# Performance work log

Measured on AMD Instinct MI355X. Metric: run time of the kernel, lower is better.

The kernel has to match this reference:

```python
import jax, jax.numpy as jnp
import numpy as np

# config (matches SS2Dv2 defaults: d_model=96, d_state=16, ssm_ratio=2.0, dt_rank=auto=6, k_group=4)
DM, DI, N, K, R = 96, 192, 16, 4, 6
BSZ, H_, W_ = 1, 56, 56


def setup_inputs() -> dict:
    key = jax.random.key(0)
    ks = jax.random.split(key, 8)
    return {
        "x": jax.random.normal(ks[0], (BSZ, H_, W_, DM), jnp.float32),
        "in_proj_w": jax.random.normal(ks[1], (2 * DI, DM), jnp.float32) / np.sqrt(DM).astype(np.float32),
        "conv_w": jax.random.normal(ks[2], (DI, 1, 3, 3), jnp.float32) * 0.1,
        "conv_b": jnp.zeros((DI,), jnp.float32),
        "x_proj_w": jax.random.normal(ks[3], (K, R + 2 * N, DI), jnp.float32) / np.sqrt(DI).astype(np.float32),
        "dt_projs_w": 0.1 * jax.random.uniform(ks[4], (K, DI, R), jnp.float32),
        "dt_projs_bias": 0.1 * jax.random.uniform(ks[5], (K, DI), jnp.float32),
        "A_logs": jnp.zeros((K * DI, N), jnp.float32),
        "Ds": jnp.ones((K * DI,), jnp.float32),
        "ln_w": jnp.ones((DI,), jnp.float32),
        "ln_b": jnp.zeros((DI,), jnp.float32),
        "out_proj_w": jax.random.normal(ks[6], (DM, DI), jnp.float32) / np.sqrt(DI).astype(np.float32),
    }


def _cross_scan(x):
    # x: (B, D, H, W) -> (B, 4, D, L); dirs: row-major, col-major, and their flips
    B, D, H, W = x.shape
    L = H * W
    x0 = x.reshape(B, D, L)
    x1 = jnp.swapaxes(x, 2, 3).reshape(B, D, L)
    return jnp.stack([x0, x1, x0[..., ::-1], x1[..., ::-1]], axis=1)


def _cross_merge(ys, H, W):
    # ys: (B, K, D, L) -> (B, D, L); invert each scan direction and sum
    B, Kk, D, L = ys.shape
    y0 = ys[:, 0]
    y2 = ys[:, 2][..., ::-1]
    y1 = jnp.swapaxes(ys[:, 1].reshape(B, D, W, H), 2, 3).reshape(B, D, L)
    y3 = jnp.swapaxes(ys[:, 3][..., ::-1].reshape(B, D, W, H), 2, 3).reshape(B, D, L)
    return y0 + y1 + y2 + y3


def _forward(x, in_proj_w, conv_w, conv_b, x_proj_w, dt_projs_w, dt_projs_bias,
             A_logs, Ds, ln_w, ln_b, out_proj_w):
    B, H, W, _ = x.shape
    L = H * W
    # in_proj + gate split (channel_first=False -> last dim)
    xz = jnp.einsum('bhwc,oc->bhwo', x, in_proj_w)
    xc, z = jnp.split(xz, 2, axis=-1)
    z = jax.nn.silu(z)
    # depthwise conv (NCHW)
    xc = jnp.transpose(xc, (0, 3, 1, 2))
    xc = jax.lax.conv_general_dilated(
        xc, conv_w, (1, 1), 'SAME', feature_group_count=DI,
        dimension_numbers=('NCHW', 'OIHW', 'NCHW')) + conv_b[None, :, None, None]
    xc = jax.nn.silu(xc)
    # 4-directional cross scan
    xs = _cross_scan(xc)  # (B,K,D,L)
    # grouped x_proj: per direction D -> R+2N
    x_dbl = jnp.einsum('bkdl,krd->bkrl', xs, x_proj_w)
    dts, Bs, Cs = jnp.split(x_dbl, [R, R + N], axis=2)  # (B,K,R,L),(B,K,N,L),(B,K,N,L)
    # grouped dt proj: per direction R -> D
    dts = jnp.einsum('bkrl,kdr->bkdl', dts, dt_projs_w)
    A = -jnp.exp(A_logs.astype(jnp.float32)).reshape(K, DI, N)
    delta = jax.nn.softplus(dts + dt_projs_bias[None, :, :, None])  # (B,K,D,L)
    # S6 selective scan: h_t = exp(delta*A)*h_{t-1} + delta*B*u, y_t = C.h_t + D*u
    dA = jnp.exp(jnp.einsum('bkdl,kdn->bkdln', delta, A))
    dBu = jnp.einsum('bkdl,bknl,bkdl->bkdln', delta, Bs, xs)

    def comb(e1, e2):
        a1, b1 = e1
        a2, b2 = e2
        return a2 * a1, a2 * b1 + b2

    _, h = jax.lax.associative_scan(comb, (dA, dBu), axis=3)  # (B,K,D,L,N)
    y = jnp.einsum('bkdln,bknl->bkdl', h, Cs) + Ds.reshape(K, DI)[None, :, :, None] * xs
    y = _cross_merge(y, H, W).reshape(B, DI, H, W)
    # out_norm: LayerNorm over channels (channel_first=False path)
    y = jnp.transpose(y, (0, 2, 3, 1))  # (B,H,W,D)
    mu = y.mean(-1, keepdims=True)
    var = ((y - mu) ** 2).mean(-1, keepdims=True)
    y = (y - mu) / jnp.sqrt(var + 1e-5) * ln_w + ln_b
    y = y * z
    return jnp.einsum('bhwd,od->bhwo', y, out_proj_w)


def reference(x, in_proj_w, conv_w, conv_b, x_proj_w, dt_projs_w, dt_projs_bias,
              A_logs, Ds, ln_w, ln_b, out_proj_w):
    return _forward(x, in_proj_w, conv_w, conv_b, x_proj_w, dt_projs_w, dt_projs_bias,
                    A_logs, Ds, ln_w, ln_b, out_proj_w)
```

## Files before the change

kernel.cpp:

```cpp
#include <hip/hip_runtime.h>
#include <hip/hip_bf16.h>
#include <math.h>

#define DM 96
#define DI 192
#define NS 16
#define KK 4
#define RR 6
#define HH 56
#define WW 56
#define LL (HH*WW)
#define RN (RR + 2*NS)
#define NCH 64
#define CLL (LL/NCH)

__device__ __forceinline__ float silu_f(float x) { return x / (1.f + __expf(-x)); }
__device__ __forceinline__ float softplus_f(float x) {
    return (x > 20.f) ? x : log1pf(__expf(x));
}

__global__ __launch_bounds__(256) void k_inproj(
        const float* __restrict__ x, const float* __restrict__ w,
        float* __restrict__ xc_t, float* __restrict__ z_nat) {
    __shared__ float xt[32 * 100];
    __shared__ float wt[32 * 100];
    const int l0 = blockIdx.x * 32;
    const int o0 = blockIdx.y * 32;
    const int tid = threadIdx.x;
    for (int i = tid; i < 32 * 24; i += 256) {
        int r = i / 24, q = i % 24;
        *(float4*)&xt[r * 100 + 4 * q] = *(const float4*)&x[(size_t)(l0 + r) * DM + 4 * q];
        *(float4*)&wt[r * 100 + 4 * q] = *(const float4*)&w[(size_t)(o0 + r) * DM + 4 * q];
    }
    __syncthreads();
    const int tx = tid & 15, ty = tid >> 4;
    float acc[2][2] = {};
    for (int c = 0; c < 96; c += 4) {
        float4 av[2], bv[2];
#pragma unroll
        for (int i = 0; i < 2; ++i) av[i] = *(const float4*)&xt[(ty + 16 * i) * 100 + c];
#pragma unroll
        for (int j = 0; j < 2; ++j) bv[j] = *(const float4*)&wt[(tx + 16 * j) * 100 + c];
#pragma unroll
        for (int i = 0; i < 2; ++i)
#pragma unroll
            for (int j = 0; j < 2; ++j) {
                acc[i][j] = fmaf(av[i].x, bv[j].x, acc[i][j]);
                acc[i][j] = fmaf(av[i].y, bv[j].y, acc[i][j]);
                acc[i][j] = fmaf(av[i].z, bv[j].z, acc[i][j]);
                acc[i][j] = fmaf(av[i].w, bv[j].w, acc[i][j]);
            }
    }
    __syncthreads();
    float* ot = xt;
#pragma unroll
    for (int j = 0; j < 2; ++j)
#pragma unroll
        for (int i = 0; i < 2; ++i)
            ot[(tx + 16 * j) * 65 + (ty + 16 * i)] = acc[i][j];
    __syncthreads();
    if (o0 < DI) {
        for (int i = tid; i < 32 * 32; i += 256) {
            int ol = i >> 5, ll = i & 31;
            xc_t[(size_t)(o0 + ol) * LL + l0 + ll] = ot[ol * 65 + ll];
        }
    } else {
        for (int i = tid; i < 32 * 32; i += 256) {
            int ll = i >> 5, ol = i & 31;
            z_nat[(size_t)(l0 + ll) * DI + (o0 - DI) + ol] = silu_f(ot[ol * 65 + ll]);
        }
    }
}

__global__ __launch_bounds__(256) void k_convT(
        const float* __restrict__ xc_t, const float* __restrict__ cw,
        const float* __restrict__ cb, float* __restrict__ xconv, float* __restrict__ xs1) {
    __shared__ float in_s[16 * 56];
    __shared__ float out_s[14 * 57];
    const int d = blockIdx.x;
    const int h0 = blockIdx.y * 14;
    const int tid = threadIdx.x;
    const float* in = xc_t + (size_t)d * LL;
    for (int i = tid; i < 16 * 14; i += 256) {
        int row = i / 14, q = i % 14;
        int r = row - 1 + h0;
        float4 v = make_float4(0.f, 0.f, 0.f, 0.f);
        if (r >= 0 && r < HH) v = *(const float4*)&in[r * WW + 4 * q];
        *(float4*)&in_s[row * 56 + 4 * q] = v;
    }
    __syncthreads();
    const float b0 = cb[d];
    float w9[9];
#pragma unroll
    for (int i = 0; i < 9; ++i) w9[i] = cw[d * 9 + i];
    for (int i = tid; i < 14 * 56; i += 256) {
        int hh = i / 56, w = i % 56;
        float acc = b0;
#pragma unroll
        for (int di = 0; di < 3; ++di)
#pragma unroll
            for (int dj = 0; dj < 3; ++dj) {
                int w2 = w + dj - 1;
                if (w2 < 0 || w2 >= WW) continue;
                acc = fmaf(in_s[(hh + di) * 56 + w2], w9[di * 3 + dj], acc);
            }
        acc = silu_f(acc);
        xconv[(size_t)d * LL + (h0 + hh) * WW + w] = acc;
        out_s[hh * 57 + w] = acc;
    }
    __syncthreads();
    for (int i = tid; i < 14 * 56; i += 256) {
        int w = i / 14, hh = i % 14;
        xs1[(size_t)d * LL + w * HH + h0 + hh] = out_s[hh * 57 + w];
    }
}

__global__ __launch_bounds__(256) void k_xdblD(
        const float* __restrict__ xconv, const float* __restrict__ xs1,
        const float* __restrict__ pw, const float* __restrict__ dtw,
        const float* __restrict__ dtb,
        float* __restrict__ Bn, float* __restrict__ Cn, float* __restrict__ delta) {
    __shared__ float xt[DI * 16];
    __shared__ float wk_s[32 * DI];
    __shared__ float dtS[RR * 17];
    const int k = blockIdx.y;
    const int l0 = blockIdx.x * 16;
    const int tid = threadIdx.x;
    const float* in = (k & 1) ? xs1 : xconv;
    const float* wk = pw + (size_t)k * RN * DI;
    for (int i = tid; i < DI * 4; i += 256) {
        int d = i >> 2, q = i & 3;
        *(float4*)&xt[(d << 4) + 4 * q] = *(const float4*)&in[(size_t)d * LL + l0 + 4 * q];
    }
    {
        const float4* src = (const float4*)(wk + RR * DI);
        float4* dst = (float4*)wk_s;
        for (int i = tid; i < (32 * DI) / 4; i += 256) dst[i] = src[i];
    }
    __syncthreads();
    if (tid < RR * 16) {
        int r = tid >> 4, lx = tid & 15;
        const float* wr = wk + r * DI;
        float acc = 0.f;
#pragma unroll 8
        for (int d = 0; d < DI; ++d) acc = fmaf(xt[(d << 4) + lx], wr[d], acc);
        dtS[r * 17 + lx] = acc;
    }
    {
        const int sx = tid & 15, cg = tid >> 4;
        float acc2[2] = {};
        for (int d = 0; d < DI; d += 4) {
            float x0 = xt[(d + 0) * 16 + sx];
            float x1 = xt[(d + 1) * 16 + sx];
            float x2 = xt[(d + 2) * 16 + sx];
            float x3 = xt[(d + 3) * 16 + sx];
#pragma unroll
            for (int j = 0; j < 2; ++j) {
                float4 wv = *(const float4*)&wk_s[(cg + 16 * j) * DI + d];
                acc2[j] = fmaf(x0, wv.x, acc2[j]);
                acc2[j] = fmaf(x1, wv.y, acc2[j]);
                acc2[j] = fmaf(x2, wv.z, acc2[j]);
                acc2[j] = fmaf(x3, wv.w, acc2[j]);
            }
        }
        int s = l0 + sx;
        Bn[((size_t)k * LL + s) * NS + cg] = acc2[0];
        Cn[((size_t)k * LL + s) * NS + cg] = acc2[1];
    }
    __syncthreads();
    for (int oi = tid; oi < DI * 16; oi += 256) {
        int d = oi >> 4, sl = oi & 15;
        int kd = k * DI + d;
        const float* wr = dtw + (size_t)kd * RR;
        float acc = dtb[kd];
#pragma unroll
        for (int r = 0; r < RR; ++r) acc = fmaf(dtS[r * 17 + sl], wr[r], acc);
        delta[(size_t)kd * LL + l0 + sl] = softplus_f(acc);
    }
}

template<int STP, bool TRANS>
__device__ __forceinline__ void scan_dir(
        const float* __restrict__ pd, const float* __restrict__ pu,
        const float* __restrict__ pB, const float* __restrict__ pC,
        float4 An, float Dv, int c, int n,
        float* __restrict__ sP, float* __restrict__ sH,
        float* __restrict__ yo0,
        float* __restrict__ ysm,
        int im0) {
    float sd = 0.f;
    float4 h = make_float4(0.f, 0.f, 0.f, 0.f);
#pragma unroll 7
    for (int tl = 0; tl < CLL; ++tl) {
        float dl = pd[STP * tl];
        float u  = pu[STP * tl];
        float4 Bv = *(const float4*)&pB[STP * NS * tl];
        float du = dl * u;
        h.x = fmaf(__builtin_amdgcn_exp2f(dl * An.x), h.x, du * Bv.x);
        h.y = fmaf(__builtin_amdgcn_exp2f(dl * An.y), h.y, du * Bv.y);
        h.z = fmaf(__builtin_amdgcn_exp2f(dl * An.z), h.z, du * Bv.z);
        h.w = fmaf(__builtin_amdgcn_exp2f(dl * An.w), h.w, du * Bv.w);
        sd += dl;
    }
    *(float4*)&sP[c * NS + 4 * n] = make_float4(
        __builtin_amdgcn_exp2f(sd * An.x), __builtin_amdgcn_exp2f(sd * An.y),
        __builtin_amdgcn_exp2f(sd * An.z), __builtin_amdgcn_exp2f(sd * An.w));
    *(float4*)&sH[c * NS + 4 * n] = h;
    __syncthreads();
    float4 hin = make_float4(0.f, 0.f, 0.f, 0.f);
    for (int cc = 0; cc < c; ++cc) {
        float4 P  = *(const float4*)&sP[cc * NS + 4 * n];
        float4 Hh = *(const float4*)&sH[cc * NS + 4 * n];
        hin.x = fmaf(P.x, hin.x, Hh.x);
        hin.y = fmaf(P.y, hin.y, Hh.y);
        hin.z = fmaf(P.z, hin.z, Hh.z);
        hin.w = fmaf(P.w, hin.w, Hh.w);
    }

    float4 h2 = hin;
    float yreg[13];
#pragma unroll 7
    for (int tl = 0; tl < CLL; ++tl) {
        float dl = pd[STP * tl];
        float u  = pu[STP * tl];
        float4 Bv = *(const float4*)&pB[STP * NS * tl];
        float4 Cv = *(const float4*)&pC[STP * NS * tl];
        float du = dl * u;
        h2.x = fmaf(__builtin_amdgcn_exp2f(dl * An.x), h2.x, du * Bv.x);
        h2.y = fmaf(__builtin_amdgcn_exp2f(dl * An.y), h2.y, du * Bv.y);
        h2.z = fmaf(__builtin_amdgcn_exp2f(dl * An.z), h2.z, du * Bv.z);
        h2.w = fmaf(__builtin_amdgcn_exp2f(dl * An.w), h2.w, du * Bv.w);
        float acc = h2.x * Cv.x;
        acc = fmaf(h2.y, Cv.y, acc);
        acc = fmaf(h2.z, Cv.z, acc);
        acc = fmaf(h2.w, Cv.w, acc);
        acc += __shfl_xor(acc, 2, 64);
        acc += __shfl_xor(acc, 1, 64);
        acc = fmaf(Dv, u, acc);
        if ((tl & 3) == n) yreg[tl >> 2] = acc;
    }
    if (!TRANS) {
#pragma unroll
        for (int j = 0; j < 12; ++j)
            yo0[STP * (j * 4 + n)] = yreg[j];
        if (n == 0)
            yo0[STP * 48] = yreg[12];
    } else {
#pragma unroll
        for (int j = 0; j < 12; ++j) {
            int im = im0 + STP * (j * 4 + n);
            int w = im / HH, hh = im - w * HH;
            ysm[hh * 57 + w] = yreg[j];
        }
        if (n == 0) {
            int im = im0 + STP * 48;
            int w = im / HH, hh = im - w * HH;
            ysm[hh * 57 + w] = yreg[12];
        }
    }
}

__global__ __launch_bounds__(256) void k_scan(
        const float* __restrict__ delta, const float* __restrict__ Bn,
        const float* __restrict__ Cn,
        const float* __restrict__ xconv, const float* __restrict__ xs1,
        const float* __restrict__ A_logs, const float* __restrict__ Ds,
        float* __restrict__ y4) {
    __shared__ float sP[NCH * NS];
    __shared__ float sH[NCH * NS];
    __shared__ float ys[HH * 57];
    int b = blockIdx.x;
    int k = b / DI, d = b % DI;
    int tid = threadIdx.x;
    int c = tid >> 2, n = tid & 3;
    int kd = k * DI + d;
    const float LOG2E = 1.4426950408889634f;
    float4 Alg = *(const float4*)&A_logs[kd * NS + 4 * n];
    float4 An = make_float4(-__expf(Alg.x) * LOG2E, -__expf(Alg.y) * LOG2E,
                            -__expf(Alg.z) * LOG2E, -__expf(Alg.w) * LOG2E);
    float Dv = Ds[kd];
    const float* del = delta + (size_t)kd * LL;
    const float* uP  = ((k & 1) ? xs1 : xconv) + (size_t)d * LL;
    const float* Bb  = Bn + (size_t)k * LL * NS;
    const float* Cb  = Cn + (size_t)k * LL * NS;
    float* yo = y4 + (size_t)kd * LL;
    const int t0 = c * CLL;
    const int imF = t0;
    const int imR = LL - 1 - t0;
    if (k == 0) {
        scan_dir<1, false>(del + imF, uP + imF,
                           Bb + (size_t)imF * NS + 4 * n, Cb + (size_t)imF * NS + 4 * n,
                           An, Dv, c, n, sP, sH, yo + imF, nullptr, 0);
    } else if (k == 1) {
        scan_dir<1, true>(del + imF, uP + imF,
                          Bb + (size_t)imF * NS + 4 * n, Cb + (size_t)imF * NS + 4 * n,
                          An, Dv, c, n, sP, sH, nullptr, ys, imF);
    } else if (k == 2) {
        scan_dir<-1, false>(del + imR, uP + imR,
                            Bb + (size_t)imR * NS + 4 * n, Cb + (size_t)imR * NS + 4 * n,
                            An, Dv, c, n, sP, sH, yo + imR, nullptr, 0);
    } else {
        scan_dir<-1, true>(del + imR, uP + imR,
                           Bb + (size_t)imR * NS + 4 * n, Cb + (size_t)imR * NS + 4 * n,
                           An, Dv, c, n, sP, sH, nullptr, ys, imR);
    }
    if (k & 1) {
        __syncthreads();
        for (int p = tid; p < LL; p += 256)
            yo[p] = ys[p + p / WW];
    }
}

__global__ __launch_bounds__(256) void k_lnout(
        const float* __restrict__ y4, const float* __restrict__ z_nat,
        const float* __restrict__ lnw, const float* __restrict__ lnb,
        const float* __restrict__ ow, float* __restrict__ out) {
    __shared__ float yv[16 * 196];
    __shared__ float ow_s[48 * 196];
    __shared__ float mean_s[16], inv_s[16];
    const int l0 = blockIdx.x * 16;
    const int tid = threadIdx.x;
    for (int i = tid; i < DI * 4; i += 256) {
        int d = i >> 2, q = i & 3;
        size_t off = (size_t)d * LL + l0 + 4 * q;
        float4 a = *(const float4*)&y4[off];
        float4 b = *(const float4*)&y4[(size_t)DI * LL + off];
        float4 c2 = *(const float4*)&y4[(size_t)(2 * DI) * LL + off];
        float4 e = *(const float4*)&y4[(size_t)(3 * DI) * LL + off];
        int p = 4 * q;
        yv[(p + 0) * 196 + d] = a.x + b.x + c2.x + e.x;
        yv[(p + 1) * 196 + d] = a.y + b.y + c2.y + e.y;
        yv[(p + 2) * 196 + d] = a.z + b.z + c2.z + e.z;
        yv[(p + 3) * 196 + d] = a.w + b.w + c2.w + e.w;
    }
    __syncthreads();
    {
        int p = tid >> 4, e = tid & 15;
        float s1 = 0.f;
#pragma unroll
        for (int m = 0; m < 12; ++m) s1 += yv[p * 196 + e + 16 * m];
        s1 += __shfl_xor(s1, 8, 64);
        s1 += __shfl_xor(s1, 4, 64);
        s1 += __shfl_xor(s1, 2, 64);
        s1 += __shfl_xor(s1, 1, 64);
        float mean = s1 * (1.f / DI);
        float s2 = 0.f;
#pragma unroll
        for (int m = 0; m < 12; ++m) {
            float dv = yv[p * 196 + e + 16 * m] - mean;
            s2 = fmaf(dv, dv, s2);
        }
        s2 += __shfl_xor(s2, 8, 64);
        s2 += __shfl_xor(s2, 4, 64);
        s2 += __shfl_xor(s2, 2, 64);
        s2 += __shfl_xor(s2, 1, 64);
        if (e == 0) {
            mean_s[p] = mean;
            inv_s[p] = rsqrtf(s2 * (1.f / DI) + 1e-5f);
        }
    }
    __syncthreads();
    for (int i = tid; i < 16 * 48; i += 256) {
        int p = i / 48, q = i % 48;
        float4 z4 = *(const float4*)&z_nat[(size_t)(l0 + p) * DI + 4 * q];
        float4 w4 = *(const float4*)&lnw[4 * q];
        float4 b4 = *(const float4*)&lnb[4 * q];
        float4 yy = *(const float4*)&yv[p * 196 + 4 * q];
        float m = mean_s[p], iv = inv_s[p];
        yy.x = ((yy.x - m) * iv * w4.x + b4.x) * z4.x;
        yy.y = ((yy.y - m) * iv * w4.y + b4.y) * z4.y;
        yy.z = ((yy.z - m) * iv * w4.z + b4.z) * z4.z;
        yy.w = ((yy.w - m) * iv * w4.w + b4.w) * z4.w;
        *(float4*)&yv[p * 196 + 4 * q] = yy;
    }
    const int ty = tid >> 4, tx = tid & 15;
#pragma unroll
    for (int pass = 0; pass < 2; ++pass) {
        __syncthreads();
        for (int i = tid; i < 48 * 48; i += 256) {
            int o = i / 48, q = i % 48;
            *(float4*)&ow_s[o * 196 + 4 * q] =
                *(const float4*)&ow[(size_t)(pass * 48 + o) * DI + 4 * q];
        }
        __syncthreads();
        float acc[3] = {};
        for (int dd = 0; dd < DI; dd += 4) {
            float4 a0 = *(const float4*)&yv[ty * 196 + dd];
#pragma unroll
            for (int j = 0; j < 3; ++j) {
                float4 bv = *(const float4*)&ow_s[(tx + 16 * j) * 196 + dd];
                acc[j] += a0.x * bv.x + a0.y * bv.y + a0.z * bv.z + a0.w * bv.w;
            }
        }
#pragma unroll
        for (int j = 0; j < 3; ++j)
            out[(size_t)(l0 + ty) * DM + pass * 48 + tx + 16 * j] = acc[j];
    }
}

extern "C" void kernel_launch(void* const* d_in, const int* in_sizes, int n_in,
                              void* d_out, int out_size, void* d_ws, size_t ws_size,
                              hipStream_t stream) {
    const float* x    = (const float*)d_in[0];
    const float* ipw  = (const float*)d_in[1];
    const float* cw   = (const float*)d_in[2];
    const float* cb   = (const float*)d_in[3];
    const float* xpw  = (const float*)d_in[4];
    const float* dtw  = (const float*)d_in[5];
    const float* dtb  = (const float*)d_in[6];
    const float* alog = (const float*)d_in[7];
    const float* Dsp  = (const float*)d_in[8];
    const float* lnw  = (const float*)d_in[9];
    const float* lnb  = (const float*)d_in[10];
    const float* ow   = (const float*)d_in[11];
    float* out = (float*)d_out;

    float* ws     = (float*)d_ws;
    float* xc_t   = ws;
    float* z_nat  = xc_t + DI * LL;
    float* xconv  = z_nat + DI * LL;
    float* xs1    = xconv + DI * LL;
    float* Bn     = xs1 + DI * LL;
    float* Cn     = Bn + (size_t)KK * LL * NS;
    float* delta  = Cn + (size_t)KK * LL * NS;
    float* y4     = delta + (size_t)KK * DI * LL;

    k_inproj <<<dim3(LL / 32, 12), 256, 0, stream>>>(x, ipw, xc_t, z_nat);
    k_convT  <<<dim3(DI, 4), 256, 0, stream>>>(xc_t, cw, cb, xconv, xs1);
    k_xdblD  <<<dim3(LL / 16, KK), 256, 0, stream>>>(xconv, xs1, xpw, dtw, dtb, Bn, Cn, delta);
    k_scan   <<<KK * DI, 256, 0, stream>>>(delta, Bn, Cn, xconv, xs1, alog, Dsp, y4);
    k_lnout  <<<LL / 16, 256, 0, stream>>>(y4, z_nat, lnw, lnb, ow, out);
}
```

Before: 184.6 us.

## Stage delta/u in LDS and reorder B/C into chunk-interleaved layout for scan

The projection kernel now writes B and C in a layout indexed by (time-in-chunk, chunk), pre-reversed for the backward directions. This lets all 64 chunk lanes in the scan read contiguous memory at each step instead of strided rows. The scan kernel first copies the delta and u rows for its (k,d) into shared memory, then reads them from LDS during both passes. It also reuses that buffer for the transposed output, which needs an extra barrier. The cost is 25KB more LDS per block, which may lower occupancy.

```diff
diff --git a/kernel.cpp b/kernel.cpp
--- a/kernel.cpp
+++ b/kernel.cpp
@@ -164,8 +164,11 @@
             }
         }
         int s = l0 + sx;
-        Bn[((size_t)k * LL + s) * NS + cg] = acc2[0];
-        Cn[((size_t)k * LL + s) * NS + cg] = acc2[1];
+        int ss = (k < 2) ? s : (LL - 1 - s);
+        int cch = ss / CLL, ttl = ss - cch * CLL;
+        size_t idx = ((size_t)k * LL + (size_t)ttl * NCH + cch) * NS + cg;
+        Bn[idx] = acc2[0];
+        Cn[idx] = acc2[1];
     }
     __syncthreads();
     for (int oi = tid; oi < DI * 16; oi += 256) {
@@ -181,20 +184,20 @@
 
 template<int STP, bool TRANS>
 __device__ __forceinline__ void scan_dir(
-        const float* __restrict__ pd, const float* __restrict__ pu,
+        const float* sDel, const float* sU,
         const float* __restrict__ pB, const float* __restrict__ pC,
         float4 An, float Dv, int c, int n,
         float* __restrict__ sP, float* __restrict__ sH,
         float* __restrict__ yo0,
-        float* __restrict__ ysm,
+        float* ysm,
         int im0) {
     float sd = 0.f;
     float4 h = make_float4(0.f, 0.f, 0.f, 0.f);
 #pragma unroll 7
     for (int tl = 0; tl < CLL; ++tl) {
-        float dl = pd[STP * tl];
-        float u  = pu[STP * tl];
-        float4 Bv = *(const float4*)&pB[STP * NS * tl];
+        float dl = sDel[STP * tl];
+        float u  = sU[STP * tl];
+        float4 Bv = *(const float4*)&pB[(size_t)tl * (NCH * NS)];
         float du = dl * u;
         h.x = fmaf(__builtin_amdgcn_exp2f(dl * An.x), h.x, du * Bv.x);
         h.y = fmaf(__builtin_amdgcn_exp2f(dl * An.y), h.y, du * Bv.y);
@@ -221,10 +224,10 @@
     float yreg[13];
 #pragma unroll 7
     for (int tl = 0; tl < CLL; ++tl) {
-        float dl = pd[STP * tl];
-        float u  = pu[STP * tl];
-        float4 Bv = *(const float4*)&pB[STP * NS * tl];
-        float4 Cv = *(const float4*)&pC[STP * NS * tl];
+        float dl = sDel[STP * tl];
+        float u  = sU[STP * tl];
+        float4 Bv = *(const float4*)&pB[(size_t)tl * (NCH * NS)];
+        float4 Cv = *(const float4*)&pC[(size_t)tl * (NCH * NS)];
         float du = dl * u;
         h2.x = fmaf(__builtin_amdgcn_exp2f(dl * An.x), h2.x, du * Bv.x);
         h2.y = fmaf(__builtin_amdgcn_exp2f(dl * An.y), h2.y, du * Bv.y);
@@ -246,6 +249,7 @@
         if (n == 0)
             yo0[STP * 48] = yreg[12];
     } else {
+        __syncthreads();
 #pragma unroll
         for (int j = 0; j < 12; ++j) {
             int im = im0 + STP * (j * 4 + n);
@@ -266,9 +270,9 @@
         const float* __restrict__ xconv, const float* __restrict__ xs1,
         const float* __restrict__ A_logs, const float* __restrict__ Ds,
         float* __restrict__ y4) {
+    __shared__ float sbuf[2 * LL];
     __shared__ float sP[NCH * NS];
     __shared__ float sH[NCH * NS];
-    __shared__ float ys[HH * 57];
     int b = blockIdx.x;
     int k = b / DI, d = b % DI;
     int tid = threadIdx.x;
@@ -281,33 +285,40 @@
     float Dv = Ds[kd];
     const float* del = delta + (size_t)kd * LL;
     const float* uP  = ((k & 1) ? xs1 : xconv) + (size_t)d * LL;
-    const float* Bb  = Bn + (size_t)k * LL * NS;
-    const float* Cb  = Cn + (size_t)k * LL * NS;
+    {
+        const float4* s1 = (const float4*)del;
+        const float4* s2 = (const float4*)uP;
+        float4* d1 = (float4*)sbuf;
+        float4* d2 = (float4*)(sbuf + LL);
+        for (int i = tid; i < LL / 4; i += 256) {
+            d1[i] = s1[i];
+            d2[i] = s2[i];
+        }
+    }
+    __syncthreads();
+    const float* Bb = Bn + (size_t)k * LL * NS + c * NS + 4 * n;
+    const float* Cb = Cn + (size_t)k * LL * NS + c * NS + 4 * n;
     float* yo = y4 + (size_t)kd * LL;
     const int t0 = c * CLL;
     const int imF = t0;
     const int imR = LL - 1 - t0;
     if (k == 0) {
-        scan_dir<1, false>(del + imF, uP + imF,
-                           Bb + (size_t)imF * NS + 4 * n, Cb + (size_t)imF * NS + 4 * n,
+        scan_dir<1, false>(sbuf + imF, sbuf + LL + imF, Bb, Cb,
                            An, Dv, c, n, sP, sH, yo + imF, nullptr, 0);
     } else if (k == 1) {
-        scan_dir<1, true>(del + imF, uP + imF,
-                          Bb + (size_t)imF * NS + 4 * n, Cb + (size_t)imF * NS + 4 * n,
-                          An, Dv, c, n, sP, sH, nullptr, ys, imF);
+        scan_dir<1, true>(sbuf + imF, sbuf + LL + imF, Bb, Cb,
+                          An, Dv, c, n, sP, sH, nullptr, sbuf, imF);
     } else if (k == 2) {
-        scan_dir<-1, false>(del + imR, uP + imR,
-                            Bb + (size_t)imR * NS + 4 * n, Cb + (size_t)imR * NS + 4 * n,
+        scan_dir<-1, false>(sbuf + imR, sbuf + LL + imR, Bb, Cb,
                             An, Dv, c, n, sP, sH, yo + imR, nullptr, 0);
     } else {
-        scan_dir<-1, true>(del + imR, uP + imR,
-                           Bb + (size_t)imR * NS + 4 * n, Cb + (size_t)imR * NS + 4 * n,
-                           An, Dv, c, n, sP, sH, nullptr, ys, imR);
+        scan_dir<-1, true>(sbuf + imR, sbuf + LL + imR, Bb, Cb,
+                           An, Dv, c, n, sP, sH, nullptr, sbuf, imR);
     }
     if (k & 1) {
         __syncthreads();
         for (int p = tid; p < LL; p += 256)
-            yo[p] = ys[p + p / WW];
+            yo[p] = sbuf[p + p / WW];
     }
 }
 
```

After: 163.1 us, median of 2. 11.6% less time.
